# Performance work log

Hardware: AMD Instinct MI355X
Metric: run time of the kernel (lower is better)

## Reference

```python
import jax, jax.numpy as jnp
import numpy as np

D_MODEL = 1024
NUM_HEADS = 16
DEPTH = D_MODEL // NUM_HEADS
MAX_LEN = 5000


def _make_pe(d_model=D_MODEL, max_len=MAX_LEN):
    # Faithful to torch PositionalEncoding: pe shape [max_len, 1, d_model]
    position = np.arange(max_len, dtype=np.float32)[:, None]
    div_term = np.exp(np.arange(0, d_model, 2, dtype=np.float32) * (-np.log(10000.0) / d_model))
    pe = np.zeros((max_len, d_model), dtype=np.float32)
    pe[:, 0::2] = np.sin(position * div_term)
    pe[:, 1::2] = np.cos(position * div_term)
    return jnp.asarray(pe[:, None, :])  # [max_len, 1, d_model]


def setup_inputs() -> dict:
    key = jax.random.key(0)
    ks = jax.random.split(key, 11)
    B, S, D = 4, 2048, D_MODEL
    s = 1.0 / np.sqrt(D)
    inp = {
        "v": jax.random.normal(ks[0], (B, S, D), jnp.float32),
        "k": jax.random.normal(ks[1], (B, S, D), jnp.float32),
        "q": jax.random.normal(ks[2], (B, S, D), jnp.float32),
        "wq_w": jax.random.normal(ks[3], (D, D), jnp.float32) * s,
        "wq_b": jnp.zeros((D,), jnp.float32),
        "wk_w": jax.random.normal(ks[4], (D, D), jnp.float32) * s,
        "wk_b": jnp.zeros((D,), jnp.float32),
        "wv_w": jax.random.normal(ks[5], (D, D), jnp.float32) * s,
        "wv_b": jnp.zeros((D,), jnp.float32),
        "dense_w": jax.random.normal(ks[6], (D, D), jnp.float32) * s,
        "dense_b": jnp.zeros((D,), jnp.float32),
        "pe": _make_pe(),
    }
    return inp


def _split_heads(x, B):
    # [B, S, D] -> [B, H, S, depth]
    return x.reshape(B, -1, NUM_HEADS, DEPTH).transpose(0, 2, 1, 3)


def reference(v, k, q, wq_w, wq_b, wk_w, wk_b, wv_w, wv_b, dense_w, dense_b, pe):
    B = q.shape[0]
    # Faithful bug-reproduction: pe[:batch] has shape [B, 1, D], broadcast over seq.
    pe_b = pe[:B]  # [B, 1, D]
    q = q + pe_b
    k = k + pe_b
    v = v + pe_b
    # Linear layers (torch: x @ W.T + b)
    qh = _split_heads(q @ wq_w.T + wq_b, B)  # [B,H,Sq,d]
    kh = _split_heads(k @ wk_w.T + wk_b, B)  # [B,H,Sk,d]
    vh = _split_heads(v @ wv_w.T + wv_b, B)  # [B,H,Sk,d]
    scale = 1.0 / jnp.sqrt(jnp.float32(DEPTH))
    logits = jnp.einsum("bhqd,bhkd->bhqk", qh, kh) * scale
    attn = jax.nn.softmax(logits, axis=-1)
    out = jnp.einsum("bhqk,bhkd->bhqd", attn, vh)
    out = out.transpose(0, 2, 1, 3).reshape(B, -1, D_MODEL)
    return out @ dense_w.T + dense_b
```

## Files before the change

kernel.cpp:

```cpp
#include <hip/hip_runtime.h>
#include <hip/hip_bf16.h>

typedef short short8 __attribute__((ext_vector_type(8)));
typedef float f32x4 __attribute__((ext_vector_type(4)));
typedef float f32x16 __attribute__((ext_vector_type(16)));
typedef unsigned int uint4v __attribute__((ext_vector_type(4)));

#define MFMA16(a, b, c) __builtin_amdgcn_mfma_f32_16x16x32_bf16(a, b, c, 0, 0, 0)
#define MFMA32(a, b, c) __builtin_amdgcn_mfma_f32_32x32x16_bf16(a, b, c, 0, 0, 0)

typedef __attribute__((address_space(1))) const unsigned int gas_u32;
typedef __attribute__((address_space(3))) unsigned int las_u32;

__device__ inline void gll16(const void* g, void* l) {
    __builtin_amdgcn_global_load_lds((gas_u32*)g, (las_u32*)l, 16, 0, 0);
}

__device__ inline unsigned short f2bf(float f) {
    unsigned u = __builtin_bit_cast(unsigned, f);
    u += 0x7fff + ((u >> 16) & 1);
    return (unsigned short)(u >> 16);
}

__device__ inline unsigned pk_perm(float a, float b, unsigned sel) {
    unsigned r;
    asm("v_perm_b32 %0, %1, %2, %3"
        : "=v"(r)
        : "v"(__builtin_bit_cast(unsigned, b)), "v"(__builtin_bit_cast(unsigned, a)), "s"(sel));
    return r;
}

__device__ inline float exp2_fast(float x) {
#if __has_builtin(__builtin_amdgcn_exp2f)
    return __builtin_amdgcn_exp2f(x);
#else
    float r; asm("v_exp_f32 %0, %1" : "=v"(r) : "v"(x)); return r;
#endif
}

__device__ inline void pl32_swap(unsigned &a, unsigned &b) {
    asm volatile("v_permlane32_swap_b32 %0, %1" : "+v"(a), "+v"(b));
}

__global__ void pe_cast3(const float* __restrict__ q, const float* __restrict__ k,
                         const float* __restrict__ v, const float* __restrict__ pe,
                         unsigned short* __restrict__ oq, unsigned short* __restrict__ ok,
                         unsigned short* __restrict__ ov) {
    const float* x = (blockIdx.y == 0) ? q : (blockIdx.y == 1) ? k : v;
    unsigned short* o = (blockIdx.y == 0) ? oq : (blockIdx.y == 1) ? ok : ov;
    int i = blockIdx.x * 256 + threadIdx.x;
    long e = (long)i * 4;
    int b = (int)(e >> 21);
    int d = (int)(e & 1023);
    float4 xv = reinterpret_cast<const float4*>(x)[i];
    float4 pv = *reinterpret_cast<const float4*>(pe + b * 1024 + d);
    ushort4 r;
    r.x = f2bf(xv.x + pv.x); r.y = f2bf(xv.y + pv.y);
    r.z = f2bf(xv.z + pv.z); r.w = f2bf(xv.w + pv.w);
    reinterpret_cast<ushort4*>(o)[i] = r;
}

__global__ void wcast4(const float* __restrict__ w0, const float* __restrict__ w1,
                       const float* __restrict__ w2, const float* __restrict__ w3,
                       unsigned short* __restrict__ o0) {
    const float* w = (blockIdx.y == 0) ? w0 : (blockIdx.y == 1) ? w1
                   : (blockIdx.y == 2) ? w2 : w3;
    unsigned short* o = o0 + (size_t)blockIdx.y * 1024 * 1024;
    int i = blockIdx.x * 256 + threadIdx.x;
    float4 xv = reinterpret_cast<const float4*>(w)[i];
    ushort4 r;
    r.x = f2bf(xv.x); r.y = f2bf(xv.y); r.z = f2bf(xv.z); r.w = f2bf(xv.w);
    reinterpret_cast<ushort4*>(o)[i] = r;
}

template <int MODE>
__global__ __launch_bounds__(512, 2) void gemm8(const unsigned short* __restrict__ A0,
                                                const unsigned short* __restrict__ W0,
                                                const float* __restrict__ bq,
                                                const float* __restrict__ bk,
                                                const float* __restrict__ bv,
                                                void* __restrict__ oq,
                                                void* __restrict__ ok,
                                                void* __restrict__ ov,
                                                float qscale) {
    const int NT = 16;
    __shared__ __align__(16) unsigned short lsA[2][256 * 64];
    __shared__ __align__(16) unsigned short lsB[2][256 * 64];

    int z = (MODE == 3) ? blockIdx.z : 0;
    const unsigned short* A = A0 + (size_t)z * 8192 * 1024;
    const unsigned short* W = W0 + (size_t)z * 1024 * 1024;
    const float* bias = (MODE == 3) ? ((z == 0) ? bq : (z == 1) ? bk : bv) : bq;
    float scale = (MODE == 3 && z == 0) ? qscale : 1.0f;

    int tid = threadIdx.x, wave = tid >> 6, lane = tid & 63;
    int lg = lane >> 4, l15 = lane & 15;
    int wr = wave >> 2, wc = wave & 3;
    int brow = blockIdx.x * 256;
    int bcol = blockIdx.y * 256;

    int srow = tid >> 3;
    int scol = ((tid ^ srow) & 7) * 8;
    const unsigned short* pA = A + (long)(brow + srow) * 1024 + scol;
    const unsigned short* pB = W + (long)(bcol + srow) * 1024 + scol;

    f32x4 acc[8][4];
#pragma unroll
    for (int m = 0; m < 8; ++m)
#pragma unroll
        for (int n = 0; n < 4; ++n) acc[m][n] = f32x4{0.f, 0.f, 0.f, 0.f};

#define SA(t, bi, q) gll16(pA + (t) * 64 + (q) * 65536,                     \
                           (char*)lsA[bi] + ((q) * 512 + wave * 64) * 16)
#define SB(t, bi, q) gll16(pB + (t) * 64 + (q) * 65536,                     \
                           (char*)lsB[bi] + ((q) * 512 + wave * 64) * 16)

    SB(0, 0, 0); SB(0, 0, 1); SB(0, 0, 2); SB(0, 0, 3);
    SA(0, 0, 0); SA(0, 0, 2); SA(0, 0, 1); SA(0, 0, 3);
    asm volatile("s_waitcnt vmcnt(2)" ::: "memory");
    __builtin_amdgcn_s_barrier();

    int swz_ = (l15 & 7) << 4;
    for (int t = 0; t < NT; ++t) {
        int cb = t & 1, nb = cb ^ 1;
        const char* KA = (const char*)lsA[cb];
        const char* KB = (const char*)lsB[cb];
        short8 af0[4][2], af1[4][2], bf0[2][2], bf1[2][2];
        const bool st = (t < NT - 1);

#pragma unroll
        for (int m = 0; m < 4; ++m)
#pragma unroll
            for (int kk = 0; kk < 2; ++kk)
                af0[m][kk] = *(const short8*)(KA + (wr * 128 + m * 16 + l15) * 128 +
                                              (((kk * 4 + lg) << 4) ^ swz_));
#pragma unroll
        for (int n = 0; n < 2; ++n)
#pragma unroll
            for (int kk = 0; kk < 2; ++kk)
                bf0[n][kk] = *(const short8*)(KB + (wc * 64 + n * 16 + l15) * 128 +
                                              (((kk * 4 + lg) << 4) ^ swz_));
        if (st) { SB(t + 1, nb, 0); SB(t + 1, nb, 1); }
        __builtin_amdgcn_s_barrier();
        asm volatile("s_waitcnt lgkmcnt(0)" ::: "memory");
        __builtin_amdgcn_s_setprio(1);
#pragma unroll
        for (int m = 0; m < 4; ++m)
#pragma unroll
            for (int n = 0; n < 2; ++n)
#pragma unroll
                for (int kk = 0; kk < 2; ++kk)
                    acc[m][n] = MFMA16(af0[m][kk], bf0[n][kk], acc[m][n]);
        __builtin_amdgcn_s_setprio(0);
        __builtin_amdgcn_s_barrier();

#pragma unroll
        for (int n = 0; n < 2; ++n)
#pragma unroll
            for (int kk = 0; kk < 2; ++kk)
                bf1[n][kk] = *(const short8*)(KB + (wc * 64 + (n + 2) * 16 + l15) * 128 +
                                              (((kk * 4 + lg) << 4) ^ swz_));
        if (st) { SB(t + 1, nb, 2); SB(t + 1, nb, 3); }
        if (st) { asm volatile("s_waitcnt vmcnt(4)" ::: "memory"); }
        else    { asm volatile("s_waitcnt vmcnt(0)" ::: "memory"); }
        __builtin_amdgcn_s_barrier();
        asm volatile("s_waitcnt lgkmcnt(0)" ::: "memory");
        __builtin_amdgcn_s_setprio(1);
#pragma unroll
        for (int m = 0; m < 4; ++m)
#pragma unroll
            for (int n = 0; n < 2; ++n)
#pragma unroll
                for (int kk = 0; kk < 2; ++kk)
                    acc[m][n + 2] = MFMA16(af0[m][kk], bf1[n][kk], acc[m][n + 2]);
        __builtin_amdgcn_s_setprio(0);
        __builtin_amdgcn_s_barrier();

#pragma unroll
        for (int m = 0; m < 4; ++m)
#pragma unroll
            for (int kk = 0; kk < 2; ++kk)
                af1[m][kk] = *(const short8*)(KA + (wr * 128 + (m + 4) * 16 + l15) * 128 +
                                              (((kk * 4 + lg) << 4) ^ swz_));
        if (st) { SA(t + 1, nb, 0); SA(t + 1, nb, 2); }
        __builtin_amdgcn_s_barrier();
        asm volatile("s_waitcnt lgkmcnt(0)" ::: "memory");
        __builtin_amdgcn_s_setprio(1);
#pragma unroll
        for (int m = 0; m < 4; ++m)
#pragma unroll
            for (int n = 0; n < 2; ++n)
#pragma unroll
                for (int kk = 0; kk < 2; ++kk)
                    acc[m + 4][n] = MFMA16(af1[m][kk], bf0[n][kk], acc[m + 4][n]);
        __builtin_amdgcn_s_setprio(0);
        __builtin_amdgcn_s_barrier();

        if (st) {
            SA(t + 1, nb, 1); SA(t + 1, nb, 3);
            asm volatile("s_waitcnt vmcnt(2)" ::: "memory");
        }
        __builtin_amdgcn_s_barrier();
        __builtin_amdgcn_s_setprio(1);
#pragma unroll
        for (int m = 0; m < 4; ++m)
#pragma unroll
            for (int n = 0; n < 2; ++n)
#pragma unroll
                for (int kk = 0; kk < 2; ++kk)
                    acc[m + 4][n + 2] = MFMA16(af1[m][kk], bf1[n][kk], acc[m + 4][n + 2]);
        __builtin_amdgcn_s_setprio(0);
        __builtin_amdgcn_s_barrier();
    }
#undef SA
#undef SB

    void* out = (MODE == 3) ? ((z == 0) ? oq : (z == 1) ? ok : ov) : oq;
#pragma unroll
    for (int m = 0; m < 8; ++m)
#pragma unroll
        for (int n = 0; n < 4; ++n) {
            int col = bcol + wc * 64 + n * 16 + l15;
            float bv_ = bias[col];
            int row0 = brow + wr * 128 + m * 16 + lg * 4;
            if (MODE == 3 && z == 2) {
                int b = row0 >> 11, s0 = row0 & 2047;
                ushort4 pk;
                pk.x = f2bf(acc[m][n][0] + bv_);
                pk.y = f2bf(acc[m][n][1] + bv_);
                pk.z = f2bf(acc[m][n][2] + bv_);
                pk.w = f2bf(acc[m][n][3] + bv_);
                *(ushort4*)((unsigned short*)out + ((long)(b * 1024 + col)) * 2048 + s0) = pk;
            } else {
#pragma unroll
                for (int r = 0; r < 4; ++r) {
                    int row = row0 + r;
                    float v = (acc[m][n][r] + bv_) * scale;
                    if (MODE == 1) {
                        ((float*)out)[(long)row * 1024 + col] = v;
                    } else {
                        int b = row >> 11, s = row & 2047, h = col >> 6, d = col & 63;
                        ((unsigned short*)out)[(((long)(b * 16 + h) * 2048 + s) * 64 + d)] = f2bf(v);
                    }
                }
            }
        }
}

__global__ __launch_bounds__(256, 2) void attn_kernel(const unsigned short* __restrict__ Qh,
                                                      const unsigned short* __restrict__ Kh,
                                                      const unsigned short* __restrict__ Vt,
                                                      unsigned short* __restrict__ Om) {
    const int S = 2048;
    const int NT = S / 64;
    int flat = blockIdx.x;
    int nf_ = (flat & 7) * 64 + (flat >> 3);
    int qt = nf_ & 7;
    int bh = nf_ >> 3;
    int b = bh >> 4, h = bh & 15;

    int tid = threadIdx.x, wave = tid >> 6, lane = tid & 63;
    int l31 = lane & 31, hi = lane >> 5;

    __shared__ __align__(16) unsigned short Kl[3][4096];
    __shared__ __align__(16) unsigned short Vtl[3][4096];

    const unsigned short* Qb = Qh + (long)bh * S * 64;
    const unsigned short* Kb = Kh + (long)bh * S * 64;
    const unsigned short* Vb = Vt + (long)bh * 64 * S;

    int colS = ((((tid & 7) * 16) ^ (((tid >> 3) & 7) << 4)) >> 1);
    const unsigned short* srcK = Kb + (tid >> 3) * 64 + colS;
    const unsigned short* srcV = Vb + (tid >> 3) * 2048 + colS;

    short8 aq[2][4];
    {
        const unsigned short* qrow = Qb + (long)(qt * 256 + wave * 64 + l31) * 64 + hi * 8;
#pragma unroll
        for (int qf = 0; qf < 2; ++qf)
#pragma unroll
            for (int s = 0; s < 4; ++s)
                aq[qf][s] = *(const short8*)(qrow + qf * 32 * 64 + s * 16);
    }

    f32x16 oacc[2][2], lacc[2], z16;
#pragma unroll
    for (int r = 0; r < 16; ++r) {
        oacc[0][0][r] = 0.f; oacc[0][1][r] = 0.f;
        oacc[1][0][r] = 0.f; oacc[1][1][r] = 0.f;
        lacc[0][r] = 0.f; lacc[1][r] = 0.f;
        z16[r] = 0.f;
    }

    const short8 ones8 = {0x3F80, 0x3F80, 0x3F80, 0x3F80, 0x3F80, 0x3F80, 0x3F80, 0x3F80};
    const unsigned SEL = 0x07060302u;

    int rb0 = l31 * 128;
    int swz = (l31 & 7) << 4;

#define STAGE(kt, bi) do {                                              \
        const unsigned short* sk = srcK + (kt) * 4096;                  \
        gll16(sk,         (char*)Kl[bi] + wave * 1024);                 \
        gll16(sk + 2048,  (char*)Kl[bi] + 4096 + wave * 1024);          \
        const unsigned short* sv = srcV + (kt) * 64;                    \
        gll16(sv,         (char*)Vtl[bi] + wave * 1024);                \
        gll16(sv + 65536, (char*)Vtl[bi] + 4096 + wave * 1024);         \
    } while (0)

    STAGE(0, 0);
    STAGE(1, 1);

    int bi = 0, sb = 2;
    for (int kt = 0; kt < NT; ++kt) {
        if (kt == NT - 1) { asm volatile("s_waitcnt vmcnt(0)" ::: "memory"); }
        else              { asm volatile("s_waitcnt vmcnt(4)" ::: "memory"); }
        __builtin_amdgcn_s_barrier();
        if (kt < NT - 2) STAGE(kt + 2, sb);

        const char* KlC = (const char*)Kl[bi];
        const char* VlC = (const char*)Vtl[bi];

        f32x16 sacc[2][2];
        __builtin_amdgcn_s_setprio(1);
#pragma unroll
        for (int blk = 0; blk < 2; ++blk) {
            short8 kf0 = *(const short8*)(KlC + blk * 4096 + rb0 + ((16 * hi) ^ swz));
            sacc[0][blk] = MFMA32(kf0, aq[0][0], z16);
            sacc[1][blk] = MFMA32(kf0, aq[1][0], z16);
#pragma unroll
            for (int s = 1; s < 4; ++s) {
                short8 kf = *(const short8*)(KlC + blk * 4096 + rb0 + ((32 * s + 16 * hi) ^ swz));
                sacc[0][blk] = MFMA32(kf, aq[0][s], sacc[0][blk]);
                sacc[1][blk] = MFMA32(kf, aq[1][s], sacc[1][blk]);
            }
        }
        __builtin_amdgcn_s_setprio(0);

#pragma unroll
        for (int qf = 0; qf < 2; ++qf)
#pragma unroll
            for (int blk = 0; blk < 2; ++blk)
#pragma unroll
                for (int r = 0; r < 16; ++r) sacc[qf][blk][r] = exp2_fast(sacc[qf][blk][r]);

#pragma unroll
        for (int s = 0; s < 4; ++s) {
            const int blk = s >> 1, base = (s & 1) * 8;
            short8 pa[2];
#pragma unroll
            for (int qf = 0; qf < 2; ++qf) {
                unsigned q0 = pk_perm(sacc[qf][blk][base + 0], sacc[qf][blk][base + 1], SEL);
                unsigned q1 = pk_perm(sacc[qf][blk][base + 2], sacc[qf][blk][base + 3], SEL);
                unsigned q2 = pk_perm(sacc[qf][blk][base + 4], sacc[qf][blk][base + 5], SEL);
                unsigned q3 = pk_perm(sacc[qf][blk][base + 6], sacc[qf][blk][base + 7], SEL);
                pl32_swap(q0, q2);
                pl32_swap(q1, q3);
                uint4v pw; pw[0] = q0; pw[1] = q1; pw[2] = q2; pw[3] = q3;
                pa[qf] = __builtin_bit_cast(short8, pw);
            }
            __builtin_amdgcn_s_setprio(1);
#pragma unroll
            for (int dblk = 0; dblk < 2; ++dblk) {
                short8 vf = *(const short8*)(VlC + dblk * 4096 + rb0 + ((32 * s + 16 * hi) ^ swz));
                oacc[0][dblk] = MFMA32(pa[0], vf, oacc[0][dblk]);
                oacc[1][dblk] = MFMA32(pa[1], vf, oacc[1][dblk]);
            }
            lacc[0] = MFMA32(pa[0], ones8, lacc[0]);
            lacc[1] = MFMA32(pa[1], ones8, lacc[1]);
            __builtin_amdgcn_s_setprio(0);
        }
        bi = (bi == 2) ? 0 : bi + 1;
        sb = (sb == 2) ? 0 : sb + 1;
    }
#undef STAGE

#pragma unroll
    for (int qf = 0; qf < 2; ++qf) {
        float inv[16];
#pragma unroll
        for (int r = 0; r < 16; ++r) inv[r] = 1.0f / lacc[qf][r];
        int qrow0 = qt * 256 + wave * 64 + qf * 32 + 4 * hi;
#pragma unroll
        for (int dblk = 0; dblk < 2; ++dblk)
#pragma unroll
            for (int r = 0; r < 16; ++r) {
                int qrow = qrow0 + (r & 3) + 8 * (r >> 2);
                int d = h * 64 + dblk * 32 + l31;
                float v = oacc[qf][dblk][r] * inv[r];
                Om[((long)b * 2048 + qrow) * 1024 + d] = f2bf(v);
            }
    }
}

extern "C" void kernel_launch(void* const* d_in, const int* in_sizes, int n_in,
                              void* d_out, int out_size, void* d_ws, size_t ws_size,
                              hipStream_t stream) {
    const float* v_in = (const float*)d_in[0];
    const float* k_in = (const float*)d_in[1];
    const float* q_in = (const float*)d_in[2];
    const float* wq_w = (const float*)d_in[3];
    const float* wq_b = (const float*)d_in[4];
    const float* wk_w = (const float*)d_in[5];
    const float* wk_b = (const float*)d_in[6];
    const float* wv_w = (const float*)d_in[7];
    const float* wv_b = (const float*)d_in[8];
    const float* wd_w = (const float*)d_in[9];
    const float* wd_b = (const float*)d_in[10];
    const float* pe   = (const float*)d_in[11];

    const long SZ = 8192L * 1024 * 2;
    char* ws = (char*)d_ws;
    unsigned short* xq = (unsigned short*)(ws + 0);
    unsigned short* xk = (unsigned short*)(ws + SZ);
    unsigned short* xv = (unsigned short*)(ws + 2 * SZ);
    unsigned short* qh = (unsigned short*)(ws + 3 * SZ);
    unsigned short* kh = (unsigned short*)(ws + 4 * SZ);
    unsigned short* vt = (unsigned short*)(ws + 5 * SZ);
    unsigned short* wqb16 = (unsigned short*)(ws + 6 * SZ);

    pe_cast3<<<dim3(8192, 3), 256, 0, stream>>>(q_in, k_in, v_in, pe, xq, xk, xv);
    wcast4<<<dim3(1024, 4), 256, 0, stream>>>(wq_w, wk_w, wv_w, wd_w, wqb16);

    const float QSCALE = 0.125f * 1.44269504088896f;
    gemm8<3><<<dim3(32, 4, 3), 512, 0, stream>>>(
        xq, wqb16, wq_b, wk_b, wv_b, qh, kh, vt, QSCALE);

    unsigned short* om = xq;
    attn_kernel<<<512, 256, 0, stream>>>(qh, kh, vt, om);

    gemm8<1><<<dim3(32, 4, 1), 512, 0, stream>>>(
        om, wqb16 + 3L * 1024 * 1024, wd_b, nullptr, nullptr, d_out, nullptr, nullptr, 1.0f);
}
```

Measured before the change: 216.1 us.

## Use smaller-tile triple-buffered GEMM for output projection to fill more CUs

The output dense projection stops reusing the 256x256-tile gemm8 kernel, which launched only 128 blocks, and gets a dedicated 128x128-tile kernel launched with 512 blocks. The new kernel uses a 3-stage global-to-LDS pipeline with swizzled layout and maps blocks so that each XCD works on nearby rows. The goal is better CU occupancy and load balance on the 8192x1024x1024 GEMM. The trade-off is less data reuse per tile and more global traffic. gemm8 loses its MODE template and is now used only for the QKV projection.

```diff
diff --git a/kernel.cpp b/kernel.cpp
--- a/kernel.cpp
+++ b/kernel.cpp
@@ -73,7 +73,6 @@
     reinterpret_cast<ushort4*>(o)[i] = r;
 }
 
-template <int MODE>
 __global__ __launch_bounds__(512, 2) void gemm8(const unsigned short* __restrict__ A0,
                                                 const unsigned short* __restrict__ W0,
                                                 const float* __restrict__ bq,
@@ -87,11 +86,11 @@
     __shared__ __align__(16) unsigned short lsA[2][256 * 64];
     __shared__ __align__(16) unsigned short lsB[2][256 * 64];
 
-    int z = (MODE == 3) ? blockIdx.z : 0;
+    int z = blockIdx.z;
     const unsigned short* A = A0 + (size_t)z * 8192 * 1024;
     const unsigned short* W = W0 + (size_t)z * 1024 * 1024;
-    const float* bias = (MODE == 3) ? ((z == 0) ? bq : (z == 1) ? bk : bv) : bq;
-    float scale = (MODE == 3 && z == 0) ? qscale : 1.0f;
+    const float* bias = (z == 0) ? bq : (z == 1) ? bk : bv;
+    float scale = (z == 0) ? qscale : 1.0f;
 
     int tid = threadIdx.x, wave = tid >> 6, lane = tid & 63;
     int lg = lane >> 4, l15 = lane & 15;
@@ -215,7 +214,7 @@
 #undef SA
 #undef SB
 
-    void* out = (MODE == 3) ? ((z == 0) ? oq : (z == 1) ? ok : ov) : oq;
+    void* out = (z == 0) ? oq : (z == 1) ? ok : ov;
 #pragma unroll
     for (int m = 0; m < 8; ++m)
 #pragma unroll
@@ -223,7 +222,7 @@
             int col = bcol + wc * 64 + n * 16 + l15;
             float bv_ = bias[col];
             int row0 = brow + wr * 128 + m * 16 + lg * 4;
-            if (MODE == 3 && z == 2) {
+            if (z == 2) {
                 int b = row0 >> 11, s0 = row0 & 2047;
                 ushort4 pk;
                 pk.x = f2bf(acc[m][n][0] + bv_);
@@ -236,13 +235,97 @@
                 for (int r = 0; r < 4; ++r) {
                     int row = row0 + r;
                     float v = (acc[m][n][r] + bv_) * scale;
-                    if (MODE == 1) {
-                        ((float*)out)[(long)row * 1024 + col] = v;
-                    } else {
-                        int b = row >> 11, s = row & 2047, h = col >> 6, d = col & 63;
-                        ((unsigned short*)out)[(((long)(b * 16 + h) * 2048 + s) * 64 + d)] = f2bf(v);
-                    }
+                    int b = row >> 11, s = row & 2047, h = col >> 6, d = col & 63;
+                    ((unsigned short*)out)[(((long)(b * 16 + h) * 2048 + s) * 64 + d)] = f2bf(v);
                 }
+            }
+        }
+}
+
+__global__ __launch_bounds__(256, 3) void gemm_dense(const unsigned short* __restrict__ A,
+                                                     const unsigned short* __restrict__ W,
+                                                     const float* __restrict__ bias,
+                                                     float* __restrict__ out) {
+    const int NT = 32;
+    __shared__ unsigned short lsA[3][128 * 32];
+    __shared__ unsigned short lsB[3][128 * 32];
+
+    int flat = blockIdx.x;
+    int xcd = flat & 7;
+    int s = flat >> 3;
+    int brow = (xcd * 8 + (s & 7)) * 128;
+    int bcol = (s >> 3) * 128;
+
+    int tid = threadIdx.x;
+    int wave = tid >> 6, lane = tid & 63, lg = lane >> 4, l15 = lane & 15;
+    int wr = wave >> 1, wc = wave & 1;
+
+    int c0 = wave * 64 + lane, c1 = 256 + c0;
+    const unsigned short* sA0 = A + (long)(brow + (c0 >> 2)) * 1024 + ((c0 ^ (c0 >> 2)) & 3) * 8;
+    const unsigned short* sA1 = A + (long)(brow + (c1 >> 2)) * 1024 + ((c1 ^ (c1 >> 2)) & 3) * 8;
+    const unsigned short* sB0 = W + (long)(bcol + (c0 >> 2)) * 1024 + ((c0 ^ (c0 >> 2)) & 3) * 8;
+    const unsigned short* sB1 = W + (long)(bcol + (c1 >> 2)) * 1024 + ((c1 ^ (c1 >> 2)) & 3) * 8;
+
+    int cread = (lg * 16) ^ ((l15 & 3) << 4);
+
+    f32x4 acc[4][4];
+#pragma unroll
+    for (int m = 0; m < 4; ++m)
+#pragma unroll
+        for (int n = 0; n < 4; ++n) acc[m][n] = f32x4{0.f, 0.f, 0.f, 0.f};
+
+#define STG(k0, bi) do {                                                  \
+        gll16(sA0 + (k0), (char*)lsA[bi] + (wave * 64) * 16);             \
+        gll16(sA1 + (k0), (char*)lsA[bi] + (256 + wave * 64) * 16);       \
+        gll16(sB0 + (k0), (char*)lsB[bi] + (wave * 64) * 16);             \
+        gll16(sB1 + (k0), (char*)lsB[bi] + (256 + wave * 64) * 16);       \
+    } while (0)
+
+    STG(0, 0);
+    STG(32, 1);
+
+    int bi = 0, sb = 2;
+    for (int t = 0; t < NT; ++t) {
+        if (t == NT - 1) { asm volatile("s_waitcnt vmcnt(0)" ::: "memory"); }
+        else             { asm volatile("s_waitcnt vmcnt(4)" ::: "memory"); }
+        __builtin_amdgcn_s_barrier();
+        if (t < NT - 2) STG((t + 2) * 32, sb);
+
+        const char* KA = (const char*)lsA[bi];
+        const char* KB = (const char*)lsB[bi];
+        short8 af[4], bf_[4];
+#pragma unroll
+        for (int m = 0; m < 4; ++m) {
+            int row = wr * 64 + m * 16 + l15;
+            af[m] = *(const short8*)(KA + row * 64 + cread);
+        }
+#pragma unroll
+        for (int n = 0; n < 4; ++n) {
+            int col = wc * 64 + n * 16 + l15;
+            bf_[n] = *(const short8*)(KB + col * 64 + cread);
+        }
+        __builtin_amdgcn_s_setprio(1);
+#pragma unroll
+        for (int m = 0; m < 4; ++m)
+#pragma unroll
+            for (int n = 0; n < 4; ++n) acc[m][n] = MFMA16(af[m], bf_[n], acc[m][n]);
+        __builtin_amdgcn_s_setprio(0);
+
+        bi = (bi == 2) ? 0 : bi + 1;
+        sb = (sb == 2) ? 0 : sb + 1;
+    }
+#undef STG
+
+#pragma unroll
+    for (int m = 0; m < 4; ++m)
+#pragma unroll
+        for (int n = 0; n < 4; ++n) {
+            int col = bcol + wc * 64 + n * 16 + l15;
+            float bv_ = bias[col];
+#pragma unroll
+            for (int r = 0; r < 4; ++r) {
+                int row = brow + wr * 64 + m * 16 + lg * 4 + r;
+                out[(long)row * 1024 + col] = acc[m][n][r] + bv_;
             }
         }
 }
@@ -422,12 +505,12 @@
     wcast4<<<dim3(1024, 4), 256, 0, stream>>>(wq_w, wk_w, wv_w, wd_w, wqb16);
 
     const float QSCALE = 0.125f * 1.44269504088896f;
-    gemm8<3><<<dim3(32, 4, 3), 512, 0, stream>>>(
+    gemm8<<<dim3(32, 4, 3), 512, 0, stream>>>(
         xq, wqb16, wq_b, wk_b, wv_b, qh, kh, vt, QSCALE);
 
     unsigned short* om = xq;
     attn_kernel<<<512, 256, 0, stream>>>(qh, kh, vt, om);
 
-    gemm8<1><<<dim3(32, 4, 1), 512, 0, stream>>>(
-        om, wqb16 + 3L * 1024 * 1024, wd_b, nullptr, nullptr, d_out, nullptr, nullptr, 1.0f);
-}
+    gemm_dense<<<512, 256, 0, stream>>>(
+        om, wqb16 + 3L * 1024 * 1024, wd_b, (float*)d_out);
+}
```

After: 205.5 us. 4.9% less time.
